# Performance work log

Hardware: AMD Instinct MI355X
Metric: run time of the kernel (lower is better)

## Reference

```python
import jax, jax.numpy as jnp
import numpy as np

POS_T = 0.7
NEG_T = 0.3
TOTAL = 256      # total_num_samples
MAX_POS = 128    # max_pos_samples
N_ANCH = 262144
N_GT = 256
IMG_H = 1024
IMG_W = 1024


def _make_boxes(key, n, img_h, img_w, min_sz, max_sz):
    # boxes in (y1, x1, y2, x2); some anchors will fall outside the image
    kc, ks = jax.random.split(key)
    cy = jax.random.uniform(kc, (n,)) * img_h
    cx = jax.random.uniform(jax.random.fold_in(kc, 1), (n,)) * img_w
    h = min_sz + jax.random.uniform(ks, (n,)) * (max_sz - min_sz)
    w = min_sz + jax.random.uniform(jax.random.fold_in(ks, 1), (n,)) * (max_sz - min_sz)
    return jnp.stack([cy - h / 2, cx - w / 2, cy + h / 2, cx + w / 2], axis=1).astype(jnp.float32)


def setup_inputs() -> dict:
    key = jax.random.key(0)
    ka, kg = jax.random.split(key)
    anchors = _make_boxes(ka, N_ANCH, IMG_H, IMG_W, 16.0, 512.0)
    gt_bboxes = _make_boxes(kg, N_GT, IMG_H, IMG_W, 32.0, 256.0)
    # keep gt boxes inside the image
    gt_bboxes = jnp.clip(gt_bboxes, 0.0, jnp.array([IMG_H, IMG_W, IMG_H, IMG_W], jnp.float32))
    return {"anchors": anchors, "gt_bboxes": gt_bboxes, "image_h": IMG_H, "image_w": IMG_W}


def _pairwise_iou(boxes_a, boxes_b):
    # boxes_a: [N,4], boxes_b: [M,4] in (y1,x1,y2,x2)
    a = boxes_a[:, None, :]   # [N,1,4]
    b = boxes_b[None, :, :]   # [1,M,4]
    ih = jnp.clip(jnp.minimum(a[..., 2], b[..., 2]) - jnp.maximum(a[..., 0], b[..., 0]), 0.0)
    iw = jnp.clip(jnp.minimum(a[..., 3], b[..., 3]) - jnp.maximum(a[..., 1], b[..., 1]), 0.0)
    inter = ih * iw                                                  # [N,M]
    area_a = (boxes_a[:, 2] - boxes_a[:, 0]) * (boxes_a[:, 3] - boxes_a[:, 1])
    area_b = (boxes_b[:, 2] - boxes_b[:, 0]) * (boxes_b[:, 3] - boxes_b[:, 1])
    union = area_a[:, None] + area_b[None, :] - inter
    return inter / jnp.maximum(union, 1e-8)


def _forward(anchors, gt_bboxes, image_h, image_w):
    n = anchors.shape[0]
    # 1. boundary filter (kept as a mask -> fixed shapes, same semantics:
    #    out-of-image anchors get label -1 and are never sampled)
    inside = ((anchors[:, 0] >= 0) & (anchors[:, 1] >= 0) &
              (anchors[:, 2] <= image_h) & (anchors[:, 3] <= image_w))
    # 2. pairwise IoU   [N, M]
    iou = _pairwise_iou(anchors, gt_bboxes)
    max_ious = jnp.max(iou, axis=1)
    argmax_ious = jnp.argmax(iou, axis=1).astype(jnp.int32)
    # 3. threshold labeling
    labels = jnp.full((n,), -1, jnp.int32)
    labels = jnp.where(max_ious > POS_T, 1, labels)
    labels = jnp.where(max_ious < NEG_T, 0, labels)
    labels = jnp.where(inside, labels, -1)
    pos_mask = labels == 1
    neg_mask = labels == 0
    total_pos = jnp.sum(pos_mask.astype(jnp.int32))
    total_neg = jnp.sum(neg_mask.astype(jnp.int32))
    cur_pos = jnp.minimum(total_pos, MAX_POS)
    cur_neg = jnp.minimum(TOTAL - cur_pos, total_neg)
    # 5. random sampling via random-score top_k (fixed-shape analogue of
    #    tf.random_shuffle + slice)
    kp, kn = jax.random.split(jax.random.key(42))
    pos_scores = jnp.where(pos_mask, jax.random.uniform(kp, (n,)), -1.0)
    neg_scores = jnp.where(neg_mask, jax.random.uniform(kn, (n,)), -1.0)
    _, pos_idx = jax.lax.top_k(pos_scores, MAX_POS)   # original anchor ids
    _, neg_idx = jax.lax.top_k(neg_scores, TOTAL)
    # pack: first cur_pos slots are positives, next cur_neg are negatives,
    # remaining slots padded with -1 (original returns a dynamic-size concat)
    out_idx = jnp.full((TOTAL,), -1, jnp.int32)
    pslot = jnp.where(jnp.arange(MAX_POS) < cur_pos, jnp.arange(MAX_POS), TOTAL)
    out_idx = out_idx.at[pslot].set(pos_idx.astype(jnp.int32), mode='drop')
    nslot = jnp.where(jnp.arange(TOTAL) < cur_neg, cur_pos + jnp.arange(TOTAL), TOTAL)
    out_idx = out_idx.at[nslot].set(neg_idx.astype(jnp.int32), mode='drop')
    safe = jnp.clip(out_idx, 0, n - 1)
    valid = out_idx >= 0
    sel_labels = jnp.where(valid, labels[safe], -1)
    sel_gt = jnp.where(valid, argmax_ious[safe], -1)
    return out_idx, sel_labels, sel_gt, cur_pos


def reference(anchors, gt_bboxes, image_h, image_w):
    return _forward(anchors, gt_bboxes, image_h, image_w)
```

## Files before the change

kernel.cpp:

```cpp
#include <hip/hip_runtime.h>

#pragma clang fp contract(off)

#define N_ANCH   262144
#define N_GT     256
#define MAX_POSK 128
#define TOTALK   256
#define NBINS    2048
#define CAP      2048
#define BORDCAP  2048

struct TF2 { unsigned a, b; };

__host__ __device__ constexpr unsigned rotl32(unsigned v, int d) {
  return (v << d) | (v >> (32 - d));
}

__host__ __device__ constexpr TF2 tf2x32(unsigned k0, unsigned k1,
                                         unsigned x0, unsigned x1) {
  unsigned ks2 = k0 ^ k1 ^ 0x1BD11BDAu;
  x0 += k0; x1 += k1;
  x0 += x1; x1 = rotl32(x1, 13); x1 ^= x0;
  x0 += x1; x1 = rotl32(x1, 15); x1 ^= x0;
  x0 += x1; x1 = rotl32(x1, 26); x1 ^= x0;
  x0 += x1; x1 = rotl32(x1,  6); x1 ^= x0;
  x0 += k1; x1 += ks2 + 1u;
  x0 += x1; x1 = rotl32(x1, 17); x1 ^= x0;
  x0 += x1; x1 = rotl32(x1, 29); x1 ^= x0;
  x0 += x1; x1 = rotl32(x1, 16); x1 ^= x0;
  x0 += x1; x1 = rotl32(x1, 24); x1 ^= x0;
  x0 += ks2; x1 += k0 + 2u;
  x0 += x1; x1 = rotl32(x1, 13); x1 ^= x0;
  x0 += x1; x1 = rotl32(x1, 15); x1 ^= x0;
  x0 += x1; x1 = rotl32(x1, 26); x1 ^= x0;
  x0 += x1; x1 = rotl32(x1,  6); x1 ^= x0;
  x0 += k0; x1 += k1 + 3u;
  x0 += x1; x1 = rotl32(x1, 17); x1 ^= x0;
  x0 += x1; x1 = rotl32(x1, 29); x1 ^= x0;
  x0 += x1; x1 = rotl32(x1, 16); x1 ^= x0;
  x0 += x1; x1 = rotl32(x1, 24); x1 ^= x0;
  x0 += k1; x1 += ks2 + 4u;
  x0 += x1; x1 = rotl32(x1, 13); x1 ^= x0;
  x0 += x1; x1 = rotl32(x1, 15); x1 ^= x0;
  x0 += x1; x1 = rotl32(x1, 26); x1 ^= x0;
  x0 += x1; x1 = rotl32(x1,  6); x1 ^= x0;
  x0 += ks2; x1 += k0 + 5u;
  return TF2{x0, x1};
}

constexpr unsigned KP0 = tf2x32(0u, 42u, 0u, 0u).a;
constexpr unsigned KP1 = tf2x32(0u, 42u, 0u, 0u).b;
constexpr unsigned KN0 = tf2x32(0u, 42u, 0u, 1u).a;
constexpr unsigned KN1 = tf2x32(0u, 42u, 0u, 1u).b;

__device__ inline unsigned score_bits(unsigned k0, unsigned k1, unsigned i) {
  TF2 r = tf2x32(k0, k1, 0u, i);
  return r.a ^ r.b;
}

constexpr double MPOSD = (double)0.7f + 0x1p-25;
constexpr double MNEGD = (double)0.3f - 0x1p-26;
constexpr float CPF = (float)(MPOSD / (1.0 + MPOSD));
constexpr float CNF = (float)(MNEGD / (1.0 + MNEGD));

__device__ unsigned           g_packed[N_ANCH];
__device__ int                g_hist[2][NBINS];
__device__ int                g_cut[2];
__device__ int                g_curpos, g_curneg;
__device__ int                g_cnt[2];
__device__ unsigned long long g_cand[2][CAP];
__device__ int                g_nbord;
__device__ int                g_bord[BORDCAP];

__global__ void k_init() {
  int t = blockIdx.x * blockDim.x + threadIdx.x;
  if (t < 2 * NBINS) (&g_hist[0][0])[t] = 0;
  if (t == 2 * NBINS)     { g_cnt[0] = 0; g_cnt[1] = 0; g_nbord = 0; }
}

__global__ __launch_bounds__(256) void k_main(const float4* __restrict__ anchors,
                                              const float4* __restrict__ gt,
                                              const int* __restrict__ ph,
                                              const int* __restrict__ pw) {
  __shared__ float4 s_gt[N_GT];
  __shared__ float  s_ga[N_GT];
  const int tid = threadIdx.x;
  {
    float4 g = gt[tid];
    s_gt[tid] = g;
    s_ga[tid] = (g.z - g.x) * (g.w - g.y);
  }
  __syncthreads();

  const int i = blockIdx.x * 256 + tid;
  const float4 a = anchors[i];
  const float Hf = (float)(*ph);
  const float Wf = (float)(*pw);
  const bool inside = (a.x >= 0.0f) && (a.y >= 0.0f) && (a.z <= Hf) && (a.w <= Wf);
  const float A = (a.z - a.x) * (a.w - a.y);

  float mrp = -1e30f, mrn = -1e30f;
  #pragma unroll 8
  for (int j = 0; j < N_GT; ++j) {
    const float4 b = s_gt[j];
    float ih = fmaxf(fminf(a.z, b.z) - fmaxf(a.x, b.x), 0.0f);
    float iw = fmaxf(fminf(a.w, b.w) - fmaxf(a.y, b.y), 0.0f);
    float inter = ih * iw;
    float t = A + s_ga[j];
    mrp = fmaxf(mrp, __builtin_fmaf(-CPF, t, inter));
    mrn = fmaxf(mrn, __builtin_fmaf(-CNF, t, inter));
  }

  const float band = 0x1p-21f * (A + 65536.0f);
  const bool pos = mrp > band;
  const bool nny = mrn > band;
  int lab = pos ? 1 : (nny ? -1 : 0);
  if (!inside) lab = -1;

  unsigned sb = 0u;
  if (lab >= 0) {
    sb = score_bits(lab == 1 ? KP0 : KN0, lab == 1 ? KP1 : KN1, (unsigned)i);
    atomicAdd(&g_hist[lab == 1 ? 0 : 1][sb >> 21], 1);
  }
  g_packed[i] = (sb & ~511u) | (unsigned)(lab + 1);

  if (inside && (fabsf(mrp) <= band || fabsf(mrn) <= band)) {
    int b = atomicAdd(&g_nbord, 1);
    if (b < BORDCAP) g_bord[b] = i;
  }
}

__device__ int find_cut(const int* cs, const int* hist, int K) {
  if (K <= 0) return NBINS;
  int suffix = 0, c = 127;
  for (; c >= 0; --c) {
    if (suffix + cs[c] >= K) break;
    suffix += cs[c];
  }
  if (c < 0) return 0;
  for (int b = c * 16 + 15; b >= c * 16; --b) {
    suffix += hist[b];
    if (suffix >= K) return b;
  }
  return c * 16;
}

__global__ __launch_bounds__(128) void k_select(const float4* __restrict__ anchors,
                                                const float4* __restrict__ gt) {
  __shared__ int  csp[128], csn[128];
  __shared__ bool s_p[128], s_n[128];
  const int t = threadIdx.x;

  int nb = g_nbord; if (nb > BORDCAP) nb = BORDCAP;
  for (int b = 0; b < nb; ++b) {
    const int i = g_bord[b];
    const float4 a = anchors[i];
    const float A = (a.z - a.x) * (a.w - a.y);
    bool p = false, nn = false;
    for (int j = t; j < N_GT; j += 128) {
      float4 bb = gt[j];
      float ih = fmaxf(fminf(a.z, bb.z) - fmaxf(a.x, bb.x), 0.0f);
      float iw = fmaxf(fminf(a.w, bb.w) - fmaxf(a.y, bb.y), 0.0f);
      float inter = ih * iw;
      float Bar = (bb.z - bb.x) * (bb.w - bb.y);
      float uni = (A + Bar) - inter;
      double id = (double)inter, ud = (double)uni;
      p  |= (id >= MPOSD * ud);
      nn |= (id >= MNEGD * ud);
    }
    s_p[t] = p; s_n[t] = nn;
    __syncthreads();
    if (t == 0) {
      bool P = false, NN = false;
      for (int k = 0; k < 128; ++k) { P |= s_p[k]; NN |= s_n[k]; }
      int newlab = P ? 1 : (NN ? -1 : 0);
      unsigned old = g_packed[i];
      int oldlab = (int)(old & 3u) - 1;
      if (newlab != oldlab) {
        if (oldlab >= 0) atomicAdd(&g_hist[oldlab == 1 ? 0 : 1][old >> 21], -1);
        unsigned sb = 0u;
        if (newlab >= 0) {
          sb = score_bits(newlab == 1 ? KP0 : KN0, newlab == 1 ? KP1 : KN1, (unsigned)i);
          atomicAdd(&g_hist[newlab == 1 ? 0 : 1][sb >> 21], 1);
        }
        g_packed[i] = (sb & ~511u) | (unsigned)(newlab + 1);
      }
    }
    __syncthreads();
  }

  int sp = 0, sn = 0;
  for (int b = t * 16; b < t * 16 + 16; ++b) { sp += g_hist[0][b]; sn += g_hist[1][b]; }
  csp[t] = sp; csn[t] = sn;
  __syncthreads();
  if (t == 0) {
    int total_p = 0, total_n = 0;
    for (int c = 0; c < 128; ++c) { total_p += csp[c]; total_n += csn[c]; }
    int cur_pos = total_p < MAX_POSK ? total_p : MAX_POSK;
    int rem = TOTALK - cur_pos;
    int cur_neg = total_n < rem ? total_n : rem;
    g_curpos = cur_pos;
    g_curneg = cur_neg;
    g_cut[0] = find_cut(csp, g_hist[0], cur_pos);
    g_cut[1] = find_cut(csn, g_hist[1], cur_neg);
  }
}

__global__ __launch_bounds__(256) void k_compact() {
  const int i = blockIdx.x * 256 + threadIdx.x;
  const unsigned p = g_packed[i];
  const int lab0 = (int)(p & 3u);
  if (lab0 == 0) return;
  const int s = (lab0 == 2) ? 0 : 1;
  if ((int)(p >> 21) >= g_cut[s]) {
    int q = atomicAdd(&g_cnt[s], 1);
    if (q < CAP)
      g_cand[s][q] = ((unsigned long long)(p >> 9) << 32) | (unsigned)(~i);
  }
}

__global__ __launch_bounds__(1024) void k_final(int* __restrict__ out) {
  __shared__ unsigned long long keys[CAP];
  const int tid = threadIdx.x;
  const int cur_pos = g_curpos;
  const int cur_neg = g_curneg;

  for (int t = tid; t < 3 * TOTALK; t += 1024) out[t] = -1;
  if (tid == 0) out[3 * TOTALK] = cur_pos;

  int Cp = g_cnt[0]; if (Cp > CAP) Cp = CAP;
  for (int t = tid; t < Cp; t += 1024) keys[t] = g_cand[0][t];
  __syncthreads();
  for (int t = tid; t < Cp; t += 1024) {
    unsigned long long me = keys[t];
    int r = 0;
    for (int u = 0; u < Cp; ++u) r += (keys[u] > me);
    if (r < cur_pos) {
      out[r] = (int)(~(unsigned)me);
      out[TOTALK + r] = 1;
    }
  }
  __syncthreads();

  int Cn = g_cnt[1]; if (Cn > CAP) Cn = CAP;
  for (int t = tid; t < Cn; t += 1024) keys[t] = g_cand[1][t];
  __syncthreads();
  for (int t = tid; t < Cn; t += 1024) {
    unsigned long long me = keys[t];
    int r = 0;
    for (int u = 0; u < Cn; ++u) r += (keys[u] > me);
    if (r < cur_neg) {
      out[cur_pos + r] = (int)(~(unsigned)me);
      out[TOTALK + cur_pos + r] = 0;
    }
  }
}

__global__ __launch_bounds__(256) void k_argmax(const float4* __restrict__ anchors,
                                                const float4* __restrict__ gt,
                                                int* __restrict__ out) {
  __shared__ unsigned long long red[256];
  const int slot = blockIdx.x;
  const int j = threadIdx.x;
  const int idx = out[slot];
  if (idx < 0) {
    if (j == 0) out[2 * TOTALK + slot] = -1;
    return;
  }
  const float4 a = anchors[idx];
  const float4 b = gt[j];
  const float A = (a.z - a.x) * (a.w - a.y);
  const float B = (b.z - b.x) * (b.w - b.y);
  float ih = fmaxf(fminf(a.z, b.z) - fmaxf(a.x, b.x), 0.0f);
  float iw = fmaxf(fminf(a.w, b.w) - fmaxf(a.y, b.y), 0.0f);
  float inter = ih * iw;
  float uni = (A + B) - inter;
  float iou = inter / fmaxf(uni, 1e-8f);
  red[j] = ((unsigned long long)__float_as_uint(iou) << 32) | (unsigned)(~j);
  __syncthreads();
  for (int s = 128; s > 0; s >>= 1) {
    if (j < s) { if (red[j + s] > red[j]) red[j] = red[j + s]; }
    __syncthreads();
  }
  if (j == 0) out[2 * TOTALK + slot] = (int)(~(unsigned)red[0]) & 0xFF;
}

extern "C" void kernel_launch(void* const* d_in, const int* in_sizes, int n_in,
                              void* d_out, int out_size, void* d_ws, size_t ws_size,
                              hipStream_t stream) {
  (void)in_sizes; (void)n_in; (void)out_size; (void)d_ws; (void)ws_size;
  const float4* anchors = (const float4*)d_in[0];
  const float4* gt      = (const float4*)d_in[1];
  const int*    ph      = (const int*)d_in[2];
  const int*    pw      = (const int*)d_in[3];
  int*          out     = (int*)d_out;

  k_init   <<<(2 * NBINS + 256) / 256, 256, 0, stream>>>();
  k_main   <<<N_ANCH / 256, 256, 0, stream>>>(anchors, gt, ph, pw);
  k_select <<<1, 128, 0, stream>>>(anchors, gt);
  k_compact<<<N_ANCH / 256, 256, 0, stream>>>();
  k_final  <<<1, 1024, 0, stream>>>(out);
  k_argmax <<<TOTALK, 256, 0, stream>>>(anchors, gt, out);
}
```

Baseline: 115.3 us.

## Process two anchors per thread, hoist area terms, use wave ballots in select

The main IoU kernel now handles two anchors per thread. Each shared-memory GT load is reused for both anchors, and the scaled GT area terms are precomputed, so the anchor-area term is subtracted once after the loop instead of once per pair. The border-refinement kernel now processes two border anchors at a time, one per wave, and combines the per-lane flags with wave ballots instead of a shared-memory loop and two block barriers per anchor. The border tolerance is widened to cover the changed rounding, which sends more anchors to the exact double-precision recheck. The grid is halved, which lowers the number of waves available for latency hiding.

```diff
diff --git a/kernel.cpp b/kernel.cpp
--- a/kernel.cpp
+++ b/kernel.cpp
@@ -75,7 +75,32 @@
 __global__ void k_init() {
   int t = blockIdx.x * blockDim.x + threadIdx.x;
   if (t < 2 * NBINS) (&g_hist[0][0])[t] = 0;
-  if (t == 2 * NBINS)     { g_cnt[0] = 0; g_cnt[1] = 0; g_nbord = 0; }
+  if (t == 2 * NBINS) { g_cnt[0] = 0; g_cnt[1] = 0; g_nbord = 0; }
+}
+
+__device__ inline void finish_anchor(int i, float4 a, float mp, float mn,
+                                     float Hf, float Wf) {
+  const float A = (a.z - a.x) * (a.w - a.y);
+  const float mrp = mp - CPF * A;
+  const float mrn = mn - CNF * A;
+  const bool inside = (a.x >= 0.0f) && (a.y >= 0.0f) && (a.z <= Hf) && (a.w <= Wf);
+  const float band = 0x1.8p-21f * (A + 65536.0f);
+  const bool pos = mrp > band;
+  const bool nny = mrn > band;
+  int lab = pos ? 1 : (nny ? -1 : 0);
+  if (!inside) lab = -1;
+
+  unsigned sb = 0u;
+  if (lab >= 0) {
+    sb = score_bits(lab == 1 ? KP0 : KN0, lab == 1 ? KP1 : KN1, (unsigned)i);
+    atomicAdd(&g_hist[lab == 1 ? 0 : 1][sb >> 21], 1);
+  }
+  g_packed[i] = (sb & ~511u) | (unsigned)(lab + 1);
+
+  if (inside && (fabsf(mrp) <= band || fabsf(mrn) <= band)) {
+    int b = atomicAdd(&g_nbord, 1);
+    if (b < BORDCAP) g_bord[b] = i;
+  }
 }
 
 __global__ __launch_bounds__(256) void k_main(const float4* __restrict__ anchors,
@@ -83,51 +108,44 @@
                                               const int* __restrict__ ph,
                                               const int* __restrict__ pw) {
   __shared__ float4 s_gt[N_GT];
-  __shared__ float  s_ga[N_GT];
+  __shared__ float  s_tp[N_GT];
+  __shared__ float  s_tn[N_GT];
   const int tid = threadIdx.x;
   {
     float4 g = gt[tid];
     s_gt[tid] = g;
-    s_ga[tid] = (g.z - g.x) * (g.w - g.y);
-  }
-  __syncthreads();
-
-  const int i = blockIdx.x * 256 + tid;
-  const float4 a = anchors[i];
+    float B = (g.z - g.x) * (g.w - g.y);
+    s_tp[tid] = CPF * B;
+    s_tn[tid] = CNF * B;
+  }
+  __syncthreads();
+
+  const int i0 = blockIdx.x * 512 + tid;
+  const int i1 = i0 + 256;
+  const float4 a0 = anchors[i0];
+  const float4 a1 = anchors[i1];
   const float Hf = (float)(*ph);
   const float Wf = (float)(*pw);
-  const bool inside = (a.x >= 0.0f) && (a.y >= 0.0f) && (a.z <= Hf) && (a.w <= Wf);
-  const float A = (a.z - a.x) * (a.w - a.y);
-
-  float mrp = -1e30f, mrn = -1e30f;
-  #pragma unroll 8
+
+  float mp0 = -1e30f, mn0 = -1e30f, mp1 = -1e30f, mn1 = -1e30f;
+  #pragma unroll 4
   for (int j = 0; j < N_GT; ++j) {
     const float4 b = s_gt[j];
-    float ih = fmaxf(fminf(a.z, b.z) - fmaxf(a.x, b.x), 0.0f);
-    float iw = fmaxf(fminf(a.w, b.w) - fmaxf(a.y, b.y), 0.0f);
-    float inter = ih * iw;
-    float t = A + s_ga[j];
-    mrp = fmaxf(mrp, __builtin_fmaf(-CPF, t, inter));
-    mrn = fmaxf(mrn, __builtin_fmaf(-CNF, t, inter));
-  }
-
-  const float band = 0x1p-21f * (A + 65536.0f);
-  const bool pos = mrp > band;
-  const bool nny = mrn > band;
-  int lab = pos ? 1 : (nny ? -1 : 0);
-  if (!inside) lab = -1;
-
-  unsigned sb = 0u;
-  if (lab >= 0) {
-    sb = score_bits(lab == 1 ? KP0 : KN0, lab == 1 ? KP1 : KN1, (unsigned)i);
-    atomicAdd(&g_hist[lab == 1 ? 0 : 1][sb >> 21], 1);
-  }
-  g_packed[i] = (sb & ~511u) | (unsigned)(lab + 1);
-
-  if (inside && (fabsf(mrp) <= band || fabsf(mrn) <= band)) {
-    int b = atomicAdd(&g_nbord, 1);
-    if (b < BORDCAP) g_bord[b] = i;
-  }
+    const float tp = s_tp[j];
+    const float tn = s_tn[j];
+    float ih0 = fmaxf(fminf(a0.z, b.z) - fmaxf(a0.x, b.x), 0.0f);
+    float iw0 = fmaxf(fminf(a0.w, b.w) - fmaxf(a0.y, b.y), 0.0f);
+    float in0 = ih0 * iw0;
+    mp0 = fmaxf(mp0, in0 - tp);
+    mn0 = fmaxf(mn0, in0 - tn);
+    float ih1 = fmaxf(fminf(a1.z, b.z) - fmaxf(a1.x, b.x), 0.0f);
+    float iw1 = fmaxf(fminf(a1.w, b.w) - fmaxf(a1.y, b.y), 0.0f);
+    float in1 = ih1 * iw1;
+    mp1 = fmaxf(mp1, in1 - tp);
+    mn1 = fmaxf(mn1, in1 - tn);
+  }
+  finish_anchor(i0, a0, mp0, mn0, Hf, Wf);
+  finish_anchor(i1, a1, mp1, mn1, Hf, Wf);
 }
 
 __device__ int find_cut(const int* cs, const int* hist, int K) {
@@ -147,17 +165,19 @@
 
 __global__ __launch_bounds__(128) void k_select(const float4* __restrict__ anchors,
                                                 const float4* __restrict__ gt) {
-  __shared__ int  csp[128], csn[128];
-  __shared__ bool s_p[128], s_n[128];
+  __shared__ int csp[128], csn[128];
   const int t = threadIdx.x;
+  const int wid = t >> 6, lane = t & 63;
 
   int nb = g_nbord; if (nb > BORDCAP) nb = BORDCAP;
-  for (int b = 0; b < nb; ++b) {
+  for (int b = wid; b < nb; b += 2) {
     const int i = g_bord[b];
     const float4 a = anchors[i];
     const float A = (a.z - a.x) * (a.w - a.y);
     bool p = false, nn = false;
-    for (int j = t; j < N_GT; j += 128) {
+    #pragma unroll
+    for (int k = 0; k < 4; ++k) {
+      const int j = lane + 64 * k;
       float4 bb = gt[j];
       float ih = fmaxf(fminf(a.z, bb.z) - fmaxf(a.x, bb.x), 0.0f);
       float iw = fmaxf(fminf(a.w, bb.w) - fmaxf(a.y, bb.y), 0.0f);
@@ -168,12 +188,10 @@
       p  |= (id >= MPOSD * ud);
       nn |= (id >= MNEGD * ud);
     }
-    s_p[t] = p; s_n[t] = nn;
-    __syncthreads();
-    if (t == 0) {
-      bool P = false, NN = false;
-      for (int k = 0; k < 128; ++k) { P |= s_p[k]; NN |= s_n[k]; }
-      int newlab = P ? 1 : (NN ? -1 : 0);
+    unsigned long long bp = __ballot(p);
+    unsigned long long bn = __ballot(nn);
+    if (lane == 0) {
+      int newlab = bp ? 1 : (bn ? -1 : 0);
       unsigned old = g_packed[i];
       int oldlab = (int)(old & 3u) - 1;
       if (newlab != oldlab) {
@@ -186,11 +204,11 @@
         g_packed[i] = (sb & ~511u) | (unsigned)(newlab + 1);
       }
     }
-    __syncthreads();
-  }
+  }
+  __syncthreads();
 
   int sp = 0, sn = 0;
-  for (int b = t * 16; b < t * 16 + 16; ++b) { sp += g_hist[0][b]; sn += g_hist[1][b]; }
+  for (int b2 = t * 16; b2 < t * 16 + 16; ++b2) { sp += g_hist[0][b2]; sn += g_hist[1][b2]; }
   csp[t] = sp; csn[t] = sn;
   __syncthreads();
   if (t == 0) {
@@ -296,7 +314,7 @@
   int*          out     = (int*)d_out;
 
   k_init   <<<(2 * NBINS + 256) / 256, 256, 0, stream>>>();
-  k_main   <<<N_ANCH / 256, 256, 0, stream>>>(anchors, gt, ph, pw);
+  k_main   <<<N_ANCH / 512, 256, 0, stream>>>(anchors, gt, ph, pw);
   k_select <<<1, 128, 0, stream>>>(anchors, gt);
   k_compact<<<N_ANCH / 256, 256, 0, stream>>>();
   k_final  <<<1, 1024, 0, stream>>>(out);
```

Result: faster. 110.8 us (-3.9%).
